# Kernel tuning notes

Hardware: AMD Instinct MI355X
Metric: run time of the kernel (lower is better)

The kernel has to match this reference:

```python
import jax, jax.numpy as jnp
import numpy as np

B, D, H, E, C = 8192, 1024, 4096, 8, 1024


def setup_inputs() -> dict:
    key = jax.random.key(0)
    ks = jax.random.split(key, 7)
    s_d = 1.0 / np.sqrt(D)
    s_h = 1.0 / np.sqrt(H)
    return {
        "x": jax.random.normal(ks[0], (B, D), dtype=jnp.float32),
        "W1": jax.random.normal(ks[1], (E, D, H), dtype=jnp.float32) * s_d,  # fc1 per expert
        "b1": jnp.zeros((E, H), dtype=jnp.float32),
        "W2": jax.random.normal(ks[2], (E, H, C), dtype=jnp.float32) * s_h,  # fc2 per expert
        "b2": jnp.zeros((E, C), dtype=jnp.float32),
        "Wg": jax.random.normal(ks[3], (D, E), dtype=jnp.float32) * s_d,     # gating fc
        "bg": jnp.zeros((E,), dtype=jnp.float32),
    }


def reference(x, W1, b1, W2, b2, Wg, bg):
    # gating: softmax over experts
    gating_weights = jax.nn.softmax(x @ Wg + bg, axis=1)            # [B, E]
    # dense MoE: every expert on every token, batched over E
    h = jax.nn.relu(jnp.einsum('bd,edh->beh', x, W1) + b1)          # [B, E, H]
    expert_outputs = jnp.einsum('beh,ehc->bec', h, W2) + b2         # [B, E, C]
    mixture_output = jnp.einsum('be,bec->bc', gating_weights, expert_outputs)  # [B, C]
    return (mixture_output, gating_weights, expert_outputs)
```

## Files before the change

kernel.cpp:

```cpp
#include <hip/hip_runtime.h>

#define B_TOK 8192
#define D_DIM 1024
#define H_DIM 4096
#define E_NUM 8
#define C_DIM 1024

typedef unsigned short ushort_t;
typedef __attribute__((ext_vector_type(8))) short bf16x8;
typedef __attribute__((ext_vector_type(4))) float f32x4;

__device__ inline ushort_t f2bf(float f) {
    unsigned u = __float_as_uint(f);
    unsigned r = (u + 0x7fffu + ((u >> 16) & 1u)) >> 16;
    return (ushort_t)r;
}

__device__ inline void async16(const ushort_t* g, void* l) {
    __builtin_amdgcn_global_load_lds((__attribute__((address_space(1))) void*)g,
                                     (__attribute__((address_space(3))) void*)l,
                                     16, 0, 0);
}

#define FENCE() asm volatile("" ::: "memory")
#define BARRIER() do { FENCE(); __builtin_amdgcn_s_barrier(); FENCE(); } while (0)
#define WAITLGKM0() asm volatile("s_waitcnt lgkmcnt(0)" ::: "memory")
#define WAITVM4()   asm volatile("s_waitcnt vmcnt(4)" ::: "memory")


#define MFMAQ(AF, BF, mq, nq)                                                  \
  _Pragma("unroll") for (int mi = 0; mi < 4; mi++)                             \
  _Pragma("unroll") for (int ni = 0; ni < 2; ni++)                             \
  _Pragma("unroll") for (int kc = 0; kc < 2; kc++)                             \
    acc[(mq) * 4 + mi][(nq) * 2 + ni] =                                        \
        __builtin_amdgcn_mfma_f32_16x16x32_bf16(                               \
            AF[mi][kc], BF[ni][kc], acc[(mq) * 4 + mi][(nq) * 2 + ni], 0, 0, 0);

#define GROUP(AVc, BVc, stA, stB, ktc)                                         \
  {                                                                            \
    int kA = (ktc) + 64;  if (kA >= K) kA -= K;                                \
    int kB = (ktc) + 128; if (kB >= K) kB -= K;                                \
    const ushort_t* gA = pa + kA;                                              \
    const ushort_t* gB = pb + kB;                                              \
                                                        \
    _Pragma("unroll") for (int mi = 0; mi < 4; mi++)                           \
      _Pragma("unroll") for (int kc = 0; kc < 2; kc++)                         \
        af[mi][kc] = (AVc)[aBase + (mi * 16) * 8 + ck[kc]];                    \
    _Pragma("unroll") for (int ni = 0; ni < 2; ni++)                           \
      _Pragma("unroll") for (int kc = 0; kc < 2; kc++)                         \
        bq0[ni][kc] = (BVc)[bBase + (ni * 16) * 8 + ck[kc]];                   \
    async16(gA,       (stA));                                                  \
    async16(gA + R64, (stA) + 8192);                                           \
    BARRIER(); WAITLGKM0();                                                    \
    __builtin_amdgcn_s_setprio(1);                                             \
    MFMAQ(af, bq0, 0, 0);                                                      \
    __builtin_amdgcn_s_setprio(0);                                             \
    BARRIER();                                                                 \
                                                        \
    _Pragma("unroll") for (int ni = 0; ni < 2; ni++)                           \
      _Pragma("unroll") for (int kc = 0; kc < 2; kc++)                         \
        bq1[ni][kc] = (BVc)[bBase + (32 + ni * 16) * 8 + ck[kc]];              \
    async16(gA + R128,       (stA) + 16384);                                   \
    async16(gA + R128 + R64, (stA) + 16384 + 8192);                            \
    BARRIER(); WAITLGKM0();                                                    \
    __builtin_amdgcn_s_setprio(1);                                             \
    MFMAQ(af, bq1, 0, 1);                                                      \
    __builtin_amdgcn_s_setprio(0);                                             \
    BARRIER();                                                                 \
                                                        \
    _Pragma("unroll") for (int mi = 0; mi < 4; mi++)                           \
      _Pragma("unroll") for (int kc = 0; kc < 2; kc++)                         \
        af[mi][kc] = (AVc)[aBase + (64 + mi * 16) * 8 + ck[kc]];               \
    async16(gB,       (stB));                                                  \
    async16(gB + R64, (stB) + 8192);                                           \
    BARRIER(); WAITLGKM0();                                                    \
    __builtin_amdgcn_s_setprio(1);                                             \
    MFMAQ(af, bq1, 1, 1);                                                      \
    __builtin_amdgcn_s_setprio(0);                                             \
    BARRIER();                                                                 \
                                                        \
    async16(gB + R128,       (stB) + 16384);                                   \
    async16(gB + R128 + R64, (stB) + 16384 + 8192);                            \
    BARRIER();                                                                 \
    __builtin_amdgcn_s_setprio(1);                                             \
    MFMAQ(af, bq0, 1, 0);                                                      \
    __builtin_amdgcn_s_setprio(0);                                             \
    WAITVM4();                                                                 \
    BARRIER();                                                                 \
  }

__global__ __launch_bounds__(512, 2) void gemm256_fc1(
    const ushort_t* __restrict__ A, const ushort_t* __restrict__ Bt,
    const float* __restrict__ bias, ushort_t* __restrict__ outH,
    int M, int N, int K, int ldc)
{
    __shared__ __align__(16) ushort_t As[2][256 * 64];
    __shared__ __align__(16) ushort_t Bs[2][256 * 64];

    const int tid  = threadIdx.x;
    const int lane = tid & 63;
    const int w    = tid >> 6;
    const int wm   = w >> 2, wn = w & 3;
    const int m0 = blockIdx.y * 256, n0 = blockIdx.x * 256;

    const int l15 = lane & 15, l4 = lane >> 4, l7 = lane & 7;

    const int srow   = tid >> 3;
    const int schunk = (tid & 7) ^ (srow & 7);
    const size_t R64  = (size_t)64 * K;
    const size_t R128 = (size_t)128 * K;
    const ushort_t* pa = A  + (size_t)(m0 + srow) * K + schunk * 8;
    const ushort_t* pb = Bt + (size_t)(n0 + srow) * K + schunk * 8;
    char* const stA0 = (char*)&As[0][0] + tid * 16;
    char* const stA1 = (char*)&As[1][0] + tid * 16;
    char* const stB0 = (char*)&Bs[0][0] + tid * 16;
    char* const stB1 = (char*)&Bs[1][0] + tid * 16;

    const bf16x8* Av0 = (const bf16x8*)&As[0][0];
    const bf16x8* Av1 = (const bf16x8*)&As[1][0];
    const bf16x8* Bv0 = (const bf16x8*)&Bs[0][0];
    const bf16x8* Bv1 = (const bf16x8*)&Bs[1][0];
    const int aBase = (wm * 128 + l15) * 8;
    const int bBase = (wn * 64 + l15) * 8;
    const int ck[2] = { l4 ^ l7, (4 + l4) ^ l7 };

    f32x4 acc[8][4];
#pragma unroll
    for (int i = 0; i < 8; i++)
#pragma unroll
        for (int j = 0; j < 4; j++) acc[i][j] = (f32x4){0.f, 0.f, 0.f, 0.f};

    bf16x8 af[4][2], bq0[2][2], bq1[2][2];

    async16(pa,              stA0);
    async16(pa + R64,        stA0 + 8192);
    async16(pa + R128,       stA0 + 16384);
    async16(pa + R128 + R64, stA0 + 16384 + 8192);
    async16(pb,              stB0);
    async16(pb + R64,        stB0 + 8192);
    async16(pb + R128,       stB0 + 16384);
    async16(pb + R128 + R64, stB0 + 16384 + 8192);
    async16(pb + 64,              stB1);
    async16(pb + 64 + R64,        stB1 + 8192);
    async16(pb + 64 + R128,       stB1 + 16384);
    async16(pb + 64 + R128 + R64, stB1 + 16384 + 8192);
    WAITVM4();
    BARRIER();

    for (int kt = 0; kt < K; kt += 128) {
        GROUP(Av0, Bv0, stA1, stB0, kt);
        GROUP(Av1, Bv1, stA0, stB1, kt + 64);
    }

    const int colq = l15, rowq = l4 * 4;
#pragma unroll
    for (int nq = 0; nq < 2; nq++)
#pragma unroll
    for (int ni = 0; ni < 2; ni++) {
        int col = n0 + wn * 64 + nq * 32 + ni * 16 + colq;
        float bv = bias[col];
#pragma unroll
        for (int mq = 0; mq < 2; mq++)
#pragma unroll
        for (int mi = 0; mi < 4; mi++) {
            int rowb = m0 + wm * 128 + mq * 64 + mi * 16 + rowq;
#pragma unroll
            for (int r = 0; r < 4; r++) {
                float v = acc[mq * 4 + mi][nq * 2 + ni][r] + bv;
                v = v > 0.f ? v : 0.f;
                outH[(size_t)(rowb + r) * ldc + col] = f2bf(v);
            }
        }
    }
}

template <bool FC1>
__global__ __launch_bounds__(256) void gemm_bt(
    const ushort_t* __restrict__ A, const ushort_t* __restrict__ Bt,
    const float* __restrict__ bias, ushort_t* __restrict__ outH,
    float* __restrict__ outF, int M, int N, int K, int ldc)
{
    __shared__ __align__(16) ushort_t As[128 * 32];
    __shared__ __align__(16) ushort_t Bs[128 * 32];

    const int tid  = threadIdx.x;
    const int w    = tid >> 6;
    const int lane = tid & 63;
    const int wm   = w >> 1, wn = w & 1;
    const int m0 = blockIdx.y * 128, n0 = blockIdx.x * 128;

    const int o1 = w * 2048 + lane * 16;
    const int o2 = o1 + 1024;
    const int r1 = o1 >> 6;
    const int kk = (o1 & 63) >> 1;

    const ushort_t* pa = A  + (size_t)(m0 + r1) * K + kk;
    const ushort_t* pb = Bt + (size_t)(n0 + r1) * K + kk;
    const size_t rowstep = (size_t)16 * K;

    char* ldsA1 = (char*)As + o1; char* ldsA2 = (char*)As + o2;
    char* ldsB1 = (char*)Bs + o1; char* ldsB2 = (char*)Bs + o2;

    f32x4 acc[4][4];
#pragma unroll
    for (int i = 0; i < 4; i++)
#pragma unroll
        for (int j = 0; j < 4; j++) acc[i][j] = (f32x4){0.f, 0.f, 0.f, 0.f};

    const bf16x8* Asv = (const bf16x8*)As;
    const bf16x8* Bsv = (const bf16x8*)Bs;
    const int ar = (wm * 64 + (lane & 15)) * 4 + (lane >> 4);
    const int br = (wn * 64 + (lane & 15)) * 4 + (lane >> 4);

    for (int kt = 0; kt < K; kt += 32) {
        async16(pa, ldsA1);
        async16(pa + rowstep, ldsA2);
        async16(pb, ldsB1);
        async16(pb + rowstep, ldsB2);
        pa += 32; pb += 32;
        __syncthreads();

        bf16x8 af[4], bg_[4];
#pragma unroll
        for (int i = 0; i < 4; i++) af[i] = Asv[ar + i * 64];
#pragma unroll
        for (int j = 0; j < 4; j++) bg_[j] = Bsv[br + j * 64];
#pragma unroll
        for (int i = 0; i < 4; i++)
#pragma unroll
            for (int j = 0; j < 4; j++)
                acc[i][j] = __builtin_amdgcn_mfma_f32_16x16x32_bf16(
                    af[i], bg_[j], acc[i][j], 0, 0, 0);
        __syncthreads();
    }

    const int colq = lane & 15, rowq = (lane >> 4) * 4;
#pragma unroll
    for (int j = 0; j < 4; j++) {
        int col = n0 + wn * 64 + j * 16 + colq;
        float bv = bias[col];
#pragma unroll
        for (int i = 0; i < 4; i++) {
            int rowb = m0 + wm * 64 + i * 16 + rowq;
#pragma unroll
            for (int r = 0; r < 4; r++) {
                float v = acc[i][j][r] + bv;
                if (FC1) {
                    v = v > 0.f ? v : 0.f;
                    outH[(size_t)(rowb + r) * ldc + col] = f2bf(v);
                } else {
                    outF[(size_t)(rowb + r) * ldc + col] = v;
                }
            }
        }
    }
}

__global__ __launch_bounds__(256) void transpose_cvt(
    const float* __restrict__ in, ushort_t* __restrict__ out, int R, int C)
{
    __shared__ float t[32][33];
    int c0 = blockIdx.x * 32, r0 = blockIdx.y * 32;
    int tx = threadIdx.x, ty = threadIdx.y;
#pragma unroll
    for (int i = 0; i < 4; i++)
        t[ty + i * 8][tx] = in[(size_t)(r0 + ty + i * 8) * C + c0 + tx];
    __syncthreads();
#pragma unroll
    for (int i = 0; i < 4; i++)
        out[(size_t)(c0 + ty + i * 8) * R + r0 + tx] = f2bf(t[tx][ty + i * 8]);
}

__global__ __launch_bounds__(256) void cvt_bf16x4(
    const float* __restrict__ in, ushort_t* __restrict__ out)
{
    int i = blockIdx.x * 256 + threadIdx.x;
    float4 v = ((const float4*)in)[i];
    unsigned lo = (unsigned)f2bf(v.x) | ((unsigned)f2bf(v.y) << 16);
    unsigned hi = (unsigned)f2bf(v.z) | ((unsigned)f2bf(v.w) << 16);
    ((uint2*)out)[i] = make_uint2(lo, hi);
}

__global__ __launch_bounds__(256) void gating_kernel(
    const float* __restrict__ x, const float* __restrict__ Wg,
    const float* __restrict__ bg, float* __restrict__ gw)
{
    int lane = threadIdx.x & 63;
    int b = blockIdx.x * 4 + (threadIdx.x >> 6);
    const float* xr = x + (size_t)b * D_DIM;
    float acc[8] = {0, 0, 0, 0, 0, 0, 0, 0};
    for (int k = 0; k < D_DIM / 64; k++) {
        int d = k * 64 + lane;
        float xv = xr[d];
        const float4* wr = (const float4*)(Wg + (size_t)d * 8);
        float4 w0 = wr[0], w1 = wr[1];
        acc[0] += xv * w0.x; acc[1] += xv * w0.y;
        acc[2] += xv * w0.z; acc[3] += xv * w0.w;
        acc[4] += xv * w1.x; acc[5] += xv * w1.y;
        acc[6] += xv * w1.z; acc[7] += xv * w1.w;
    }
#pragma unroll
    for (int off = 32; off > 0; off >>= 1)
#pragma unroll
        for (int e = 0; e < 8; e++) acc[e] += __shfl_xor(acc[e], off, 64);

    float mx = -1e30f;
#pragma unroll
    for (int e = 0; e < 8; e++) { acc[e] += bg[e]; mx = fmaxf(mx, acc[e]); }
    float s = 0.f;
#pragma unroll
    for (int e = 0; e < 8; e++) { acc[e] = expf(acc[e] - mx); s += acc[e]; }
    float outv = acc[0];
#pragma unroll
    for (int e = 1; e < 8; e++) outv = (lane == e) ? acc[e] : outv;
    if (lane < 8) gw[(size_t)b * 8 + lane] = outv / s;
}

__global__ __launch_bounds__(256) void mixture_kernel(
    const float* __restrict__ gw, const float* __restrict__ eo,
    float* __restrict__ mix)
{
    int b = blockIdx.x, t = threadIdx.x;
    float g[8];
#pragma unroll
    for (int e = 0; e < 8; e++) g[e] = gw[(size_t)b * 8 + e];
    const float4* ep = (const float4*)(eo + (size_t)b * (E_NUM * C_DIM));
    float4 a = make_float4(0.f, 0.f, 0.f, 0.f);
#pragma unroll
    for (int e = 0; e < 8; e++) {
        float4 v = ep[e * 256 + t];
        a.x += g[e] * v.x; a.y += g[e] * v.y;
        a.z += g[e] * v.z; a.w += g[e] * v.w;
    }
    ((float4*)(mix + (size_t)b * C_DIM))[t] = a;
}

extern "C" void kernel_launch(void* const* d_in, const int* in_sizes, int n_in,
                              void* d_out, int out_size, void* d_ws,
                              size_t ws_size, hipStream_t stream)
{
    const float* x  = (const float*)d_in[0];
    const float* W1 = (const float*)d_in[1];
    const float* b1 = (const float*)d_in[2];
    const float* W2 = (const float*)d_in[3];
    const float* b2 = (const float*)d_in[4];
    const float* Wg = (const float*)d_in[5];
    const float* bg = (const float*)d_in[6];

    float* mix = (float*)d_out;
    float* gw  = mix + (size_t)B_TOK * C_DIM;
    float* eo  = gw + (size_t)B_TOK * E_NUM;

    ushort_t* xb  = (ushort_t*)d_ws;
    ushort_t* w1t = xb + (size_t)B_TOK * D_DIM;
    ushort_t* w2t = w1t + (size_t)H_DIM * D_DIM;
    ushort_t* hb  = w2t + (size_t)C_DIM * H_DIM;

    cvt_bf16x4<<<(B_TOK * D_DIM) / 1024, 256, 0, stream>>>(x, xb);
    gating_kernel<<<B_TOK / 4, 256, 0, stream>>>(x, Wg, bg, gw);

    for (int e = 0; e < E_NUM; e++) {
        transpose_cvt<<<dim3(H_DIM / 32, D_DIM / 32), dim3(32, 8), 0, stream>>>(
            W1 + (size_t)e * D_DIM * H_DIM, w1t, D_DIM, H_DIM);
        gemm256_fc1<<<dim3(H_DIM / 256, B_TOK / 256), 512, 0, stream>>>(
            xb, w1t, b1 + (size_t)e * H_DIM, hb, B_TOK, H_DIM, D_DIM, H_DIM);
        transpose_cvt<<<dim3(C_DIM / 32, H_DIM / 32), dim3(32, 8), 0, stream>>>(
            W2 + (size_t)e * H_DIM * C_DIM, w2t, H_DIM, C_DIM);
        gemm_bt<false><<<dim3(C_DIM / 128, B_TOK / 128), 256, 0, stream>>>(
            hb, w2t, b2 + (size_t)e * C_DIM, nullptr, eo + (size_t)e * C_DIM,
            B_TOK, C_DIM, H_DIM, E_NUM * C_DIM);
    }

    mixture_kernel<<<B_TOK, 256, 0, stream>>>(gw, eo, mix);
}
```

Before: 2.086 ms.

## Batch experts over grid z and use 256-tile pipelined GEMM for fc2

New measurement: 1.793 ms. -14.0%, faster.

```diff
diff --git a/kernel.cpp b/kernel.cpp
--- a/kernel.cpp
+++ b/kernel.cpp
@@ -25,7 +25,7 @@
 #define FENCE() asm volatile("" ::: "memory")
 #define BARRIER() do { FENCE(); __builtin_amdgcn_s_barrier(); FENCE(); } while (0)
 #define WAITLGKM0() asm volatile("s_waitcnt lgkmcnt(0)" ::: "memory")
-#define WAITVM4()   asm volatile("s_waitcnt vmcnt(4)" ::: "memory")
+#define WAITVM8()   asm volatile("s_waitcnt vmcnt(8)" ::: "memory")
 
 
 #define MFMAQ(AF, BF, mq, nq)                                                  \
@@ -38,64 +38,70 @@
 
 #define GROUP(AVc, BVc, stA, stB, ktc)                                         \
   {                                                                            \
-    int kA = (ktc) + 64;  if (kA >= K) kA -= K;                                \
-    int kB = (ktc) + 128; if (kB >= K) kB -= K;                                \
-    const ushort_t* gA = pa + kA;                                              \
-    const ushort_t* gB = pb + kB;                                              \
-                                                        \
+    int kN = (ktc) + 128; if (kN >= K) kN -= K;                                \
+    const ushort_t* gA = pa + kN;                                              \
+    const ushort_t* gB = pb + kN;                                              \
+                                    \
     _Pragma("unroll") for (int mi = 0; mi < 4; mi++)                           \
       _Pragma("unroll") for (int kc = 0; kc < 2; kc++)                         \
         af[mi][kc] = (AVc)[aBase + (mi * 16) * 8 + ck[kc]];                    \
     _Pragma("unroll") for (int ni = 0; ni < 2; ni++)                           \
       _Pragma("unroll") for (int kc = 0; kc < 2; kc++)                         \
         bq0[ni][kc] = (BVc)[bBase + (ni * 16) * 8 + ck[kc]];                   \
-    async16(gA,       (stA));                                                  \
-    async16(gA + R64, (stA) + 8192);                                           \
     BARRIER(); WAITLGKM0();                                                    \
     __builtin_amdgcn_s_setprio(1);                                             \
     MFMAQ(af, bq0, 0, 0);                                                      \
     __builtin_amdgcn_s_setprio(0);                                             \
     BARRIER();                                                                 \
-                                                        \
+                                            \
     _Pragma("unroll") for (int ni = 0; ni < 2; ni++)                           \
       _Pragma("unroll") for (int kc = 0; kc < 2; kc++)                         \
         bq1[ni][kc] = (BVc)[bBase + (32 + ni * 16) * 8 + ck[kc]];              \
-    async16(gA + R128,       (stA) + 16384);                                   \
-    async16(gA + R128 + R64, (stA) + 16384 + 8192);                            \
     BARRIER(); WAITLGKM0();                                                    \
     __builtin_amdgcn_s_setprio(1);                                             \
     MFMAQ(af, bq1, 0, 1);                                                      \
     __builtin_amdgcn_s_setprio(0);                                             \
     BARRIER();                                                                 \
-                                                        \
+      \
     _Pragma("unroll") for (int mi = 0; mi < 4; mi++)                           \
       _Pragma("unroll") for (int kc = 0; kc < 2; kc++)                         \
         af[mi][kc] = (AVc)[aBase + (64 + mi * 16) * 8 + ck[kc]];               \
-    async16(gB,       (stB));                                                  \
-    async16(gB + R64, (stB) + 8192);                                           \
+    async16(gB,              (stB));                                           \
+    async16(gB + R64,        (stB) + 8192);                                    \
+    async16(gB + R128,       (stB) + 16384);                                   \
+    async16(gB + R128 + R64, (stB) + 24576);                                   \
     BARRIER(); WAITLGKM0();                                                    \
     __builtin_amdgcn_s_setprio(1);                                             \
     MFMAQ(af, bq1, 1, 1);                                                      \
     __builtin_amdgcn_s_setprio(0);                                             \
     BARRIER();                                                                 \
-                                                        \
-    async16(gB + R128,       (stB) + 16384);                                   \
-    async16(gB + R128 + R64, (stB) + 16384 + 8192);                            \
+                   \
+    async16(gA,              (stA));                                           \
+    async16(gA + R64,        (stA) + 8192);                                    \
+    async16(gA + R128,       (stA) + 16384);                                   \
+    async16(gA + R128 + R64, (stA) + 24576);                                   \
     BARRIER();                                                                 \
     __builtin_amdgcn_s_setprio(1);                                             \
     MFMAQ(af, bq0, 1, 0);                                                      \
     __builtin_amdgcn_s_setprio(0);                                             \
-    WAITVM4();                                                                 \
+    WAITVM8();                                                                 \
     BARRIER();                                                                 \
   }
 
-__global__ __launch_bounds__(512, 2) void gemm256_fc1(
+template <bool RELU_BF16>
+__global__ __launch_bounds__(512, 2) void gemm256(
     const ushort_t* __restrict__ A, const ushort_t* __restrict__ Bt,
     const float* __restrict__ bias, ushort_t* __restrict__ outH,
-    int M, int N, int K, int ldc)
+    float* __restrict__ outF, int K, int ldc,
+    size_t eA, size_t eB, size_t eBias, size_t eOut)
 {
     __shared__ __align__(16) ushort_t As[2][256 * 64];
     __shared__ __align__(16) ushort_t Bs[2][256 * 64];
+
+    const int z = blockIdx.z;
+    A    += (size_t)z * eA;
+    Bt   += (size_t)z * eB;
+    bias += (size_t)z * eBias;
 
     const int tid  = threadIdx.x;
     const int lane = tid & 63;
@@ -135,21 +141,25 @@
     async16(pa,              stA0);
     async16(pa + R64,        stA0 + 8192);
     async16(pa + R128,       stA0 + 16384);
-    async16(pa + R128 + R64, stA0 + 16384 + 8192);
+    async16(pa + R128 + R64, stA0 + 24576);
     async16(pb,              stB0);
     async16(pb + R64,        stB0 + 8192);
     async16(pb + R128,       stB0 + 16384);
-    async16(pb + R128 + R64, stB0 + 16384 + 8192);
+    async16(pb + R128 + R64, stB0 + 24576);
+    async16(pa + 64,              stA1);
+    async16(pa + 64 + R64,        stA1 + 8192);
+    async16(pa + 64 + R128,       stA1 + 16384);
+    async16(pa + 64 + R128 + R64, stA1 + 24576);
     async16(pb + 64,              stB1);
     async16(pb + 64 + R64,        stB1 + 8192);
     async16(pb + 64 + R128,       stB1 + 16384);
-    async16(pb + 64 + R128 + R64, stB1 + 16384 + 8192);
-    WAITVM4();
+    async16(pb + 64 + R128 + R64, stB1 + 24576);
+    WAITVM8();
     BARRIER();
 
     for (int kt = 0; kt < K; kt += 128) {
-        GROUP(Av0, Bv0, stA1, stB0, kt);
-        GROUP(Av1, Bv1, stA0, stB1, kt + 64);
+        GROUP(Av0, Bv0, stA0, stB0, kt);
+        GROUP(Av1, Bv1, stA1, stB1, kt + 64);
     }
 
     const int colq = l15, rowq = l4 * 4;
@@ -167,18 +177,21 @@
 #pragma unroll
             for (int r = 0; r < 4; r++) {
                 float v = acc[mq * 4 + mi][nq * 2 + ni][r] + bv;
-                v = v > 0.f ? v : 0.f;
-                outH[(size_t)(rowb + r) * ldc + col] = f2bf(v);
+                if (RELU_BF16) {
+                    v = v > 0.f ? v : 0.f;
+                    (outH + (size_t)z * eOut)[(size_t)(rowb + r) * ldc + col] = f2bf(v);
+                } else {
+                    (outF + (size_t)z * eOut)[(size_t)(rowb + r) * ldc + col] = v;
+                }
             }
         }
     }
 }
 
-template <bool FC1>
-__global__ __launch_bounds__(256) void gemm_bt(
+__global__ __launch_bounds__(256) void gemm_bt_f32(
     const ushort_t* __restrict__ A, const ushort_t* __restrict__ Bt,
-    const float* __restrict__ bias, ushort_t* __restrict__ outH,
-    float* __restrict__ outF, int M, int N, int K, int ldc)
+    const float* __restrict__ bias, float* __restrict__ outF,
+    int M, int N, int K, int ldc)
 {
     __shared__ __align__(16) ushort_t As[128 * 32];
     __shared__ __align__(16) ushort_t Bs[128 * 32];
@@ -243,15 +256,8 @@
         for (int i = 0; i < 4; i++) {
             int rowb = m0 + wm * 64 + i * 16 + rowq;
 #pragma unroll
-            for (int r = 0; r < 4; r++) {
-                float v = acc[i][j][r] + bv;
-                if (FC1) {
-                    v = v > 0.f ? v : 0.f;
-                    outH[(size_t)(rowb + r) * ldc + col] = f2bf(v);
-                } else {
-                    outF[(size_t)(rowb + r) * ldc + col] = v;
-                }
-            }
+            for (int r = 0; r < 4; r++)
+                outF[(size_t)(rowb + r) * ldc + col] = acc[i][j][r] + bv;
         }
     }
 }
@@ -260,6 +266,9 @@
     const float* __restrict__ in, ushort_t* __restrict__ out, int R, int C)
 {
     __shared__ float t[32][33];
+    size_t zoff = (size_t)blockIdx.z * R * C;
+    in  += zoff;
+    out += zoff;
     int c0 = blockIdx.x * 32, r0 = blockIdx.y * 32;
     int tx = threadIdx.x, ty = threadIdx.y;
 #pragma unroll
@@ -351,24 +360,52 @@
     float* gw  = mix + (size_t)B_TOK * C_DIM;
     float* eo  = gw + (size_t)B_TOK * E_NUM;
 
-    ushort_t* xb  = (ushort_t*)d_ws;
-    ushort_t* w1t = xb + (size_t)B_TOK * D_DIM;
-    ushort_t* w2t = w1t + (size_t)H_DIM * D_DIM;
-    ushort_t* hb  = w2t + (size_t)C_DIM * H_DIM;
-
-    cvt_bf16x4<<<(B_TOK * D_DIM) / 1024, 256, 0, stream>>>(x, xb);
+    const size_t nXB  = (size_t)B_TOK * D_DIM;
+    const size_t nW1e = (size_t)H_DIM * D_DIM;
+    const size_t nW2e = (size_t)C_DIM * H_DIM;
+    const size_t nHBe = (size_t)B_TOK * H_DIM;
+
+    const size_t needBig = (nXB + 8 * nW1e + 8 * nW2e + 8 * nHBe) * sizeof(ushort_t);
+
+    cvt_bf16x4<<<(B_TOK * D_DIM) / 1024, 256, 0, stream>>>(x, (ushort_t*)d_ws);
     gating_kernel<<<B_TOK / 4, 256, 0, stream>>>(x, Wg, bg, gw);
 
-    for (int e = 0; e < E_NUM; e++) {
-        transpose_cvt<<<dim3(H_DIM / 32, D_DIM / 32), dim3(32, 8), 0, stream>>>(
-            W1 + (size_t)e * D_DIM * H_DIM, w1t, D_DIM, H_DIM);
-        gemm256_fc1<<<dim3(H_DIM / 256, B_TOK / 256), 512, 0, stream>>>(
-            xb, w1t, b1 + (size_t)e * H_DIM, hb, B_TOK, H_DIM, D_DIM, H_DIM);
-        transpose_cvt<<<dim3(C_DIM / 32, H_DIM / 32), dim3(32, 8), 0, stream>>>(
-            W2 + (size_t)e * H_DIM * C_DIM, w2t, H_DIM, C_DIM);
-        gemm_bt<false><<<dim3(C_DIM / 128, B_TOK / 128), 256, 0, stream>>>(
-            hb, w2t, b2 + (size_t)e * C_DIM, nullptr, eo + (size_t)e * C_DIM,
-            B_TOK, C_DIM, H_DIM, E_NUM * C_DIM);
+    if (ws_size >= needBig) {
+        ushort_t* xb     = (ushort_t*)d_ws;
+        ushort_t* w1tAll = xb + nXB;
+        ushort_t* w2tAll = w1tAll + 8 * nW1e;
+        ushort_t* hbAll  = w2tAll + 8 * nW2e;
+
+        transpose_cvt<<<dim3(H_DIM / 32, D_DIM / 32, 8), dim3(32, 8), 0, stream>>>(
+            W1, w1tAll, D_DIM, H_DIM);
+        transpose_cvt<<<dim3(C_DIM / 32, H_DIM / 32, 8), dim3(32, 8), 0, stream>>>(
+            W2, w2tAll, H_DIM, C_DIM);
+
+        gemm256<true><<<dim3(H_DIM / 256, B_TOK / 256, 8), 512, 0, stream>>>(
+            xb, w1tAll, b1, hbAll, nullptr, D_DIM, H_DIM,
+            0, nW1e, H_DIM, nHBe);
+
+        gemm256<false><<<dim3(C_DIM / 256, B_TOK / 256, 8), 512, 0, stream>>>(
+            hbAll, w2tAll, b2, nullptr, eo, H_DIM, E_NUM * C_DIM,
+            nHBe, nW2e, C_DIM, C_DIM);
+    } else {
+        ushort_t* xb  = (ushort_t*)d_ws;
+        ushort_t* w1t = xb + nXB;
+        ushort_t* w2t = w1t + nW1e;
+        ushort_t* hb  = w2t + nW2e;
+
+        for (int e = 0; e < E_NUM; e++) {
+            transpose_cvt<<<dim3(H_DIM / 32, D_DIM / 32, 1), dim3(32, 8), 0, stream>>>(
+                W1 + (size_t)e * D_DIM * H_DIM, w1t, D_DIM, H_DIM);
+            gemm256<true><<<dim3(H_DIM / 256, B_TOK / 256, 1), 512, 0, stream>>>(
+                xb, w1t, b1 + (size_t)e * H_DIM, hb, nullptr, D_DIM, H_DIM,
+                0, 0, 0, 0);
+            transpose_cvt<<<dim3(C_DIM / 32, H_DIM / 32, 1), dim3(32, 8), 0, stream>>>(
+                W2 + (size_t)e * H_DIM * C_DIM, w2t, H_DIM, C_DIM);
+            gemm_bt_f32<<<dim3(C_DIM / 128, B_TOK / 128), 256, 0, stream>>>(
+                hb, w2t, b2 + (size_t)e * C_DIM, eo + (size_t)e * C_DIM,
+                B_TOK, C_DIM, H_DIM, E_NUM * C_DIM);
+        }
     }
 
     mixture_kernel<<<B_TOK, 256, 0, stream>>>(gw, eo, mix);
```
